# Performance work log

Measured on AMD Instinct MI355X. Metric: run time of the kernel, lower is better.

The kernel has to match this reference:

```python
import jax, jax.numpy as jnp
import numpy as np
from jax.scipy.special import digamma, gammaln

NUM_CLASSES = 3
FOCAL_GAMMA = 2.0
LABEL_SMOOTHING = 0.1
EVIDENTIAL_W = 0.1
CONTRASTIVE_W = 0.1
BOUNDARY_W = 0.15
TRIPLET_W = 0.1
QUALITY_W = 0.1
TRIPLET_MARGIN = 1.5


def setup_inputs() -> dict:
    key = jax.random.key(0)
    k1, k2, k3 = jax.random.split(key, 3)
    B, D = 4096, 512
    logits = jax.random.normal(k1, (B, NUM_CLASSES), dtype=jnp.float32)
    targets = jax.random.randint(k2, (B,), 0, 3)
    features = jax.random.normal(k3, (B, D), dtype=jnp.float32)
    alpha = jax.random.uniform(jax.random.fold_in(key, 7), (B, NUM_CLASSES), dtype=jnp.float32)
    focal_alpha = jnp.array([1.0, 2.0, 1.5], dtype=jnp.float32)
    class_weights = jnp.array([1.0, 2.0, 1.5], dtype=jnp.float32)
    return {"logits": logits, "targets": targets, "features": features,
            "alpha": alpha, "epoch": 1, "focal_alpha": focal_alpha,
            "class_weights": class_weights}


def reference(logits, targets, features, alpha, epoch, focal_alpha, class_weights):
    B = logits.shape[0]
    C = NUM_CLASSES

    # ---- focal loss (label-smoothed CE, torch semantics) ----
    logp = jax.nn.log_softmax(logits, axis=1)                      # [B,C]
    nll = -jnp.take_along_axis(logp, targets[:, None], axis=1)[:, 0]
    ce_ls = (1.0 - LABEL_SMOOTHING) * nll + LABEL_SMOOTHING * (-logp.mean(axis=1))
    pt = jnp.exp(-ce_ls)
    focal = (focal_alpha[targets] * (1.0 - pt) ** FOCAL_GAMMA * ce_ls).mean()

    # ---- weighted CE (torch weighted mean: sum(w*nll)/sum(w)) ----
    w = class_weights[targets]
    ce = (w * nll).sum() / w.sum()

    # ---- enhanced boundary loss ----
    probs = jax.nn.softmax(logits, axis=1)
    real = targets == 0
    semi = targets == 1
    syn = targets == 2
    rb = jnp.where(real, probs[:, 1] + 0.6 * probs[:, 2], 0.0).sum()
    sb = jnp.where(syn, probs[:, 1] + 0.4 * probs[:, 0], 0.0).sum()
    mb = jnp.where(semi, 1.0 - probs[:, 1] + 0.3 * (probs[:, 0] + probs[:, 2]), 0.0).sum()
    boundary = (rb + sb + 4.5 * mb) / (B + 1e-8)

    total = 0.4 * focal + 0.3 * ce + BOUNDARY_W * boundary

    # ---- normalized features and pairwise cosine-sim matrix ----
    norms = jnp.linalg.norm(features, axis=1, keepdims=True)
    f = features / jnp.maximum(norms, 1e-12)
    sim = f @ f.T                                                  # [B,B]
    same = targets[:, None] == targets[None, :]
    eye = jnp.eye(B, dtype=bool)

    # ---- enhanced contrastive loss ----
    pos = jnp.where(same, (1.0 - sim) ** 2, 0.0).sum()
    neg = jnp.where(~same, jnp.clip(sim - 0.2, 0.0) ** 2, 0.0).sum()
    semi_pair = semi[:, None] & semi[None, :]
    semi_l = jnp.where(semi_pair, (1.0 - sim) ** 2, 0.0).sum()
    contrastive = (pos + neg + 4.0 * semi_l) / (B * B + 1e-8)

    # ---- enhanced triplet loss (batch-hard, vectorized) ----
    d2 = jnp.clip(2.0 - 2.0 * sim, 0.0)
    dist = jnp.sqrt(jnp.where(eye, 1.0, d2))  # diag masked; safe sqrt
    pos_mask = same & ~eye
    neg_mask = ~same
    hp = jnp.max(jnp.where(pos_mask, dist, -jnp.inf), axis=1)
    hn = jnp.min(jnp.where(neg_mask, dist, jnp.inf), axis=1)
    valid = pos_mask.any(axis=1) & neg_mask.any(axis=1)
    margin = TRIPLET_MARGIN * jnp.where(targets == 1, 2.5, 1.0)
    tl = jax.nn.relu(hp - hn + margin)
    cnt = valid.sum()
    triplet = jnp.where(cnt > 0,
                        jnp.where(valid, tl, 0.0).sum() / jnp.maximum(cnt, 1),
                        0.0)

    # ---- quality-invariant loss (upper-tri same-class pairs) ----
    upper = jnp.triu(jnp.ones((B, B), dtype=bool), k=1)
    qmask = same & upper
    npairs = qmask.sum()
    q = jnp.where(qmask, (1.0 - sim) ** 2, 0.0).sum() / jnp.maximum(npairs, 1)
    frac2 = syn.astype(jnp.float32).mean()
    q = q * jnp.where(syn.sum() > 0, 1.0 + 2.5 * frac2, 1.0)
    quality = jnp.where(npairs > 0, q, 0.0)

    # ---- evidential loss ----
    onehot = jax.nn.one_hot(targets, C, dtype=jnp.float32)
    S = alpha.sum(axis=1, keepdims=True) + 1e-8
    likelihood = (onehot * (digamma(S) - digamma(alpha + 1e-8))).sum(axis=1)
    at = onehot + (1.0 - onehot) * alpha
    ats = at.sum(axis=1) + 1e-8
    kl = (gammaln(ats) - gammaln(at + 1e-8).sum(axis=1)
          + ((at - 1.0) * (digamma(at + 1e-8) - digamma(ats[:, None] + 1e-8))).sum(axis=1))
    annealing = min(1.0, (epoch / 25.0) ** 2)
    evidential = likelihood.mean() + annealing * 0.2 * kl.mean()

    total = (total + CONTRASTIVE_W * contrastive + TRIPLET_W * triplet
             + QUALITY_W * quality + EVIDENTIAL_W * evidential)
    return total
```

## Files before the change

### kernel.cpp

```cpp
#include <hip/hip_runtime.h>
#include <hip/hip_bf16.h>
#include <cstdint>

typedef __attribute__((ext_vector_type(8))) __bf16 bf8;
typedef __attribute__((ext_vector_type(4))) float f32x4;

#if defined(__has_builtin)
#if __has_builtin(__builtin_amdgcn_global_load_lds)
#define USE_GLL 1
#endif
#endif
#ifndef USE_GLL
#define USE_GLL 0
#endif

#if USE_GLL
__device__ __forceinline__ void gll16(const __bf16* g, __bf16* l){
  __builtin_amdgcn_global_load_lds(
      (const __attribute__((address_space(1))) void*)g,
      (__attribute__((address_space(3))) void*)l, 16, 0, 0);
}
#endif

__device__ __forceinline__ unsigned mapf(float x){
  unsigned u = __float_as_uint(x);
  return (u & 0x80000000u) ? ~u : (u | 0x80000000u);
}
__device__ __forceinline__ float unmapf(unsigned u){
  return __uint_as_float((u & 0x80000000u) ? (u & 0x7FFFFFFFu) : ~u);
}

__device__ float digammaf_(float x){
  float r = 0.f;
  while (x < 6.f){ r -= 1.f/x; x += 1.f; }
  float inv = 1.f/x, inv2 = inv*inv;
  r += logf(x) - 0.5f*inv
     - inv2*(0.08333333333f - inv2*(0.008333333333f - inv2*0.003968253968f));
  return r;
}

__global__ __launch_bounds__(256) void k_prep(const float* __restrict__ feat,
    __bf16* __restrict__ fb,
    const float* __restrict__ logits, const int* __restrict__ targets,
    const float* __restrict__ alpha,  const float* __restrict__ fa,
    const float* __restrict__ cw, int B, int D,
    float* __restrict__ psum, unsigned* __restrict__ pcnt,
    unsigned* rowMinU, unsigned* rowMaxU){
  int bid = blockIdx.x, tid = threadIdx.x;
  int wave = tid >> 6, lane = tid & 63;

  int row = bid*4 + wave;
  if (row < B){
    const float* src = feat + (size_t)row*D;
    float ss = 0.f;
    for (int c = lane*4; c < D; c += 64*4){
      float4 v = *(const float4*)(src + c);
      ss += v.x*v.x + v.y*v.y + v.z*v.z + v.w*v.w;
    }
    #pragma unroll
    for (int off=32; off; off>>=1) ss += __shfl_xor(ss, off);
    float inv = 1.f / fmaxf(sqrtf(ss), 1e-12f);
    __bf16* dst = fb + (size_t)row*D;
    for (int c = lane*8; c < D; c += 64*8){
      float4 v0 = *(const float4*)(src + c);
      float4 v1 = *(const float4*)(src + c + 4);
      bf8 o;
      o[0]=(__bf16)(v0.x*inv); o[1]=(__bf16)(v0.y*inv);
      o[2]=(__bf16)(v0.z*inv); o[3]=(__bf16)(v0.w*inv);
      o[4]=(__bf16)(v1.x*inv); o[5]=(__bf16)(v1.y*inv);
      o[6]=(__bf16)(v1.z*inv); o[7]=(__bf16)(v1.w*inv);
      *(bf8*)(dst + c) = o;
    }
  }

  int SB = B >> 8;
  if (bid >= SB) return;

  int i = bid*256 + tid;
  rowMinU[i] = 0xFFFFFFFFu; rowMaxU[i] = 0u;

  float l0=logits[3*i], l1=logits[3*i+1], l2=logits[3*i+2];
  int t = targets[i];
  float m = fmaxf(l0, fmaxf(l1,l2));
  float e0=expf(l0-m), e1=expf(l1-m), e2=expf(l2-m);
  float se = e0+e1+e2;
  float lse = m + logf(se);
  float lp0=l0-lse, lp1=l1-lse, lp2=l2-lse;
  float lpt = (t==0)?lp0:((t==1)?lp1:lp2);
  float nll = -lpt;
  float ce_ls = 0.9f*nll + 0.1f*(-(lp0+lp1+lp2)*(1.f/3.f));
  float pt = expf(-ce_ls);
  float om = 1.f - pt;
  float focal_i = fa[t]*om*om*ce_ls;
  float w = cw[t];
  float ce_n = w*nll, ce_d = w;
  float p0=e0/se, p1=e1/se, p2=e2/se;
  float bnd;
  if (t==0)      bnd = p1 + 0.6f*p2;
  else if (t==2) bnd = p1 + 0.4f*p0;
  else           bnd = 4.5f*(1.f - p1 + 0.3f*(p0+p2));
  float a0=alpha[3*i], a1=alpha[3*i+1], a2=alpha[3*i+2];
  float S = a0+a1+a2 + 1e-8f;
  float at_ = (t==0)?a0:((t==1)?a1:a2);
  float lik = digammaf_(S) - digammaf_(at_ + 1e-8f);
  float b0 = (t==0)?1.f:a0, b1 = (t==1)?1.f:a1, b2 = (t==2)?1.f:a2;
  float ats = b0+b1+b2 + 1e-8f;
  float psa = digammaf_(ats + 1e-8f);
  float kl = lgammaf(ats)
     - (lgammaf(b0+1e-8f)+lgammaf(b1+1e-8f)+lgammaf(b2+1e-8f))
     + (b0-1.f)*(digammaf_(b0+1e-8f)-psa)
     + (b1-1.f)*(digammaf_(b1+1e-8f)-psa)
     + (b2-1.f)*(digammaf_(b2+1e-8f)-psa);

  unsigned long long m0 = __ballot(t==0);
  unsigned long long m1 = __ballot(t==1);
  unsigned long long m2 = __ballot(t==2);
  #pragma unroll
  for (int off=32; off; off>>=1){
    focal_i += __shfl_xor(focal_i, off);
    ce_n    += __shfl_xor(ce_n, off);
    ce_d    += __shfl_xor(ce_d, off);
    bnd     += __shfl_xor(bnd, off);
    lik     += __shfl_xor(lik, off);
    kl      += __shfl_xor(kl, off);
  }
  if (lane == 0){
    int slot = bid*4 + wave;
    psum[slot*8+0]=focal_i; psum[slot*8+1]=ce_n; psum[slot*8+2]=ce_d;
    psum[slot*8+3]=bnd;     psum[slot*8+4]=lik;  psum[slot*8+5]=kl;
    pcnt[slot*4+0]=(unsigned)__popcll(m0);
    pcnt[slot*4+1]=(unsigned)__popcll(m1);
    pcnt[slot*4+2]=(unsigned)__popcll(m2);
  }
}

__global__ __launch_bounds__(64, 3) void k_pairs(const __bf16* __restrict__ fb,
    const int* __restrict__ targets, int B, int D,
    float* __restrict__ pairPart, unsigned* rowMinU, unsigned* rowMaxU){
  __shared__ __bf16 sA[2][2048];
  __shared__ __bf16 sB[2][2048];

  int t = blockIdx.x;
  int bx = (int)((sqrtf(8.f*(float)t + 1.f) - 1.f)*0.5f);
  while ((bx+1)*(bx+2)/2 <= t) bx++;
  while (bx*(bx+1)/2 > t) bx--;
  int by = t - bx*(bx+1)/2;
  bool isDiag = (by == bx);
  int rowBase = by*64, colBase = bx*64;

  int lane = threadIdx.x;
  int quad = lane >> 4, l16 = lane & 15;

  const __bf16* gA[4]; const __bf16* gB[4];
  #pragma unroll
  for (int j=0; j<4; j++){
    int row = j*16 + (lane >> 2);
    int gcb = (lane & 3) ^ ((row >> 1) & 3);
    gA[j] = fb + (size_t)(rowBase + row)*D + gcb*8;
    gB[j] = fb + (size_t)(colBase + row)*D + gcb*8;
  }

  int offA[4], offB[4];
  #pragma unroll
  for (int mi=0; mi<4; mi++){
    int R = mi*16 + l16;
    offA[mi] = R*32 + ((quad ^ ((R>>1)&3))*8);
    offB[mi] = offA[mi];
  }

  f32x4 C[4][4] = {};

#if USE_GLL
  #define STAGE(buf, k0) do{ \
    gll16(gA[0] + (k0), &sA[buf][0*512]); \
    gll16(gA[1] + (k0), &sA[buf][1*512]); \
    gll16(gA[2] + (k0), &sA[buf][2*512]); \
    gll16(gA[3] + (k0), &sA[buf][3*512]); \
    gll16(gB[0] + (k0), &sB[buf][0*512]); \
    gll16(gB[1] + (k0), &sB[buf][1*512]); \
    gll16(gB[2] + (k0), &sB[buf][2*512]); \
    gll16(gB[3] + (k0), &sB[buf][3*512]); \
  }while(0)
#else
  #define STAGE(buf, k0) do{ \
    _Pragma("unroll") \
    for (int j=0; j<4; j++){ \
      *(bf8*)&sA[buf][j*512 + lane*8] = *(const bf8*)(gA[j] + (k0)); \
      *(bf8*)&sB[buf][j*512 + lane*8] = *(const bf8*)(gB[j] + (k0)); \
    } \
  }while(0)
#endif

  #define COMPUTE(buf) do{ \
    bf8 aF[4], bF[4]; \
    _Pragma("unroll") \
    for (int mi=0; mi<4; mi++) aF[mi] = *(const bf8*)(&sA[buf][offA[mi]]); \
    _Pragma("unroll") \
    for (int ni=0; ni<4; ni++) bF[ni] = *(const bf8*)(&sB[buf][offB[ni]]); \
    _Pragma("unroll") \
    for (int mi=0; mi<4; mi++) \
      _Pragma("unroll") \
      for (int ni=0; ni<4; ni++) \
        C[mi][ni] = __builtin_amdgcn_mfma_f32_16x16x32_bf16(aF[mi], bF[ni], C[mi][ni], 0,0,0); \
  }while(0)

  int NIT = D/32;
  STAGE(0, 0);
  for (int it=0; it<NIT; it+=2){
    STAGE(1, (it+1)*32);
    COMPUTE(0);
    if (it+2 < NIT) STAGE(0, (it+2)*32);
    COMPUTE(1);
  }

  int tcol[4];
  #pragma unroll
  for (int ni=0; ni<4; ni++) tcol[ni] = targets[colBase + ni*16 + l16];

  float pos=0.f, neg=0.f, semi=0.f, diag=0.f;
  float cmin[4], cmax[4];
  #pragma unroll
  for (int ni=0; ni<4; ni++){ cmin[ni]=2.f; cmax[ni]=-2.f; }

  #pragma unroll
  for (int mi=0; mi<4; mi++){
    #pragma unroll
    for (int r=0; r<4; r++){
      int rl = mi*16 + quad*4 + r;
      int row = rowBase + rl;
      int tr = targets[row];
      float vmin = 2.f, vmax = -2.f;
      #pragma unroll
      for (int ni=0; ni<4; ni++){
        int col = colBase + ni*16 + l16;
        float s = C[mi][ni][r];
        if (tr == tcol[ni]){
          float omv = 1.f - s;
          float q = omv*omv;
          pos += q;
          if (tr == 1) semi += q;
          if (row == col) diag += q;
          else {
            vmin = fminf(vmin, s);
            cmin[ni] = fminf(cmin[ni], s);
          }
        } else {
          float c0 = fmaxf(s - 0.2f, 0.f);
          neg += c0*c0;
          vmax = fmaxf(vmax, s);
          cmax[ni] = fmaxf(cmax[ni], s);
        }
      }
      #pragma unroll
      for (int off=1; off<16; off<<=1){
        vmin = fminf(vmin, __shfl_xor(vmin, off));
        vmax = fmaxf(vmax, __shfl_xor(vmax, off));
      }
      if (l16 == 0){
        atomicMin(&rowMinU[row], mapf(vmin));
        atomicMax(&rowMaxU[row], mapf(vmax));
      }
    }
  }

  if (!isDiag){
    #pragma unroll
    for (int ni=0; ni<4; ni++){
      float cn = cmin[ni], cx = cmax[ni];
      cn = fminf(cn, __shfl_xor(cn, 16)); cn = fminf(cn, __shfl_xor(cn, 32));
      cx = fmaxf(cx, __shfl_xor(cx, 16)); cx = fmaxf(cx, __shfl_xor(cx, 32));
      if (quad == 0){
        int col = colBase + ni*16 + l16;
        atomicMin(&rowMinU[col], mapf(cn));
        atomicMax(&rowMaxU[col], mapf(cx));
      }
    }
  }

  #pragma unroll
  for (int off=32; off; off>>=1){
    pos  += __shfl_xor(pos, off);
    neg  += __shfl_xor(neg, off);
    semi += __shfl_xor(semi, off);
    diag += __shfl_xor(diag, off);
  }
  if (lane == 0){
    float fac = isDiag ? 1.f : 2.f;
    pairPart[blockIdx.x*4+0] = pos*fac;
    pairPart[blockIdx.x*4+1] = neg*fac;
    pairPart[blockIdx.x*4+2] = semi*fac;
    pairPart[blockIdx.x*4+3] = diag;
  }
}

__global__ __launch_bounds__(256) void k_final(const int* __restrict__ targets,
    const int* __restrict__ epoch_p, int B, int SB, int nblk,
    const float* __restrict__ pairPart, const float* __restrict__ psum,
    const unsigned* __restrict__ pcnt,
    const unsigned* rowMinU, const unsigned* rowMaxU, float* out){
  __shared__ float tot[6];
  __shared__ unsigned cn[3];
  __shared__ float ptot[4];
  int tid = threadIdx.x;
  int nslots = SB*4;
  int wave = tid>>6, lane = tid&63;

  if (tid < 64){
    float v0=0,v1=0,v2=0,v3=0,v4=0,v5=0;
    int c0=0,c1=0,c2=0;
    for (int s=tid; s<nslots; s+=64){
      v0+=psum[s*8+0]; v1+=psum[s*8+1]; v2+=psum[s*8+2];
      v3+=psum[s*8+3]; v4+=psum[s*8+4]; v5+=psum[s*8+5];
      c0+=(int)pcnt[s*4+0]; c1+=(int)pcnt[s*4+1]; c2+=(int)pcnt[s*4+2];
    }
    #pragma unroll
    for (int off=32; off; off>>=1){
      v0+=__shfl_xor(v0,off); v1+=__shfl_xor(v1,off); v2+=__shfl_xor(v2,off);
      v3+=__shfl_xor(v3,off); v4+=__shfl_xor(v4,off); v5+=__shfl_xor(v5,off);
      c0+=__shfl_xor(c0,off); c1+=__shfl_xor(c1,off); c2+=__shfl_xor(c2,off);
    }
    if (tid == 0){
      tot[0]=v0; tot[1]=v1; tot[2]=v2; tot[3]=v3; tot[4]=v4; tot[5]=v5;
      cn[0]=(unsigned)c0; cn[1]=(unsigned)c1; cn[2]=(unsigned)c2;
    }
  }

  {
    float p=0,n=0,s2=0,d=0;
    for (int s=tid; s<nblk; s+=256){
      p += pairPart[s*4+0]; n += pairPart[s*4+1];
      s2+= pairPart[s*4+2]; d += pairPart[s*4+3];
    }
    #pragma unroll
    for (int off=32; off; off>>=1){
      p+=__shfl_xor(p,off); n+=__shfl_xor(n,off);
      s2+=__shfl_xor(s2,off); d+=__shfl_xor(d,off);
    }
    __shared__ float pw[4][4];
    if (lane==0){ pw[wave][0]=p; pw[wave][1]=n; pw[wave][2]=s2; pw[wave][3]=d; }
    __syncthreads();
    if (tid==0){
      float a=0,b=0,c=0,e=0;
      for (int w2=0; w2<4; w2++){ a+=pw[w2][0]; b+=pw[w2][1]; c+=pw[w2][2]; e+=pw[w2][3]; }
      ptot[0]=a; ptot[1]=b; ptot[2]=c; ptot[3]=e;
    }
  }
  __syncthreads();
  int n0=(int)cn[0], n1=(int)cn[1], n2=(int)cn[2];

  float tsum = 0.f, tcnt = 0.f;
  for (int i = tid; i < B; i += 256){
    int t = targets[i];
    int nt = (t==0)?n0:((t==1)?n1:n2);
    if (nt - 1 > 0 && B - nt > 0){
      float mn = unmapf(rowMinU[i]);
      float mx = unmapf(rowMaxU[i]);
      float hp = sqrtf(fmaxf(2.f - 2.f*mn, 0.f));
      float hn = sqrtf(fmaxf(2.f - 2.f*mx, 0.f));
      float margin = 1.5f * ((t==1) ? 2.5f : 1.f);
      float tl = fmaxf(hp - hn + margin, 0.f);
      tsum += tl; tcnt += 1.f;
    }
  }
  #pragma unroll
  for (int off=32; off; off>>=1){ tsum += __shfl_xor(tsum, off); tcnt += __shfl_xor(tcnt, off); }
  __shared__ float sb[4][2];
  if (lane==0){ sb[wave][0]=tsum; sb[wave][1]=tcnt; }
  __syncthreads();
  if (tid==0){
    float ts=0, tn=0;
    for (int w2=0;w2<4;w2++){ ts+=sb[w2][0]; tn+=sb[w2][1]; }
    float triplet = (tn > 0.f) ? ts / fmaxf(tn, 1.f) : 0.f;
    float pos=ptot[0], neg=ptot[1], semi=ptot[2], diag=ptot[3];
    float Bf = (float)B;
    float focal = tot[0] / Bf;
    float ce = tot[1] / tot[2];
    float boundary = tot[3] / (Bf + 1e-8f);
    float contrastive = (pos + neg + 4.f*semi) / (Bf*Bf + 1e-8f);
    long long npl = ((long long)n0*(n0-1) + (long long)n1*(n1-1) + (long long)n2*(n2-1))/2;
    float qsum = (pos - diag) * 0.5f;
    float q = qsum / (float)(npl > 0 ? npl : 1);
    if (n2 > 0) q *= (1.f + 2.5f * ((float)n2 / Bf));
    float quality = (npl > 0) ? q : 0.f;
    int ep = epoch_p[0];
    float er = (float)ep / 25.f;
    float ann = fminf(1.f, er*er);
    float evidential = tot[4]/Bf + ann*0.2f*tot[5]/Bf;
    float total = 0.4f*focal + 0.3f*ce + 0.15f*boundary
                + 0.1f*contrastive + 0.1f*triplet + 0.1f*quality + 0.1f*evidential;
    out[0] = total;
  }
}

extern "C" void kernel_launch(void* const* d_in, const int* in_sizes, int n_in,
                              void* d_out, int out_size, void* d_ws, size_t ws_size,
                              hipStream_t stream){
  const float* logits   = (const float*)d_in[0];
  const int*   targets  = (const int*)d_in[1];
  const float* features = (const float*)d_in[2];
  const float* alpha    = (const float*)d_in[3];
  const int*   epoch    = (const int*)d_in[4];
  const float* fa       = (const float*)d_in[5];
  const float* cw       = (const float*)d_in[6];
  int B = in_sizes[1];
  int D = in_sizes[2] / B;
  int SB = B >> 8;
  int T  = B / 64;
  int nblk = T*(T+1)/2;

  char* ws = (char*)d_ws;
  unsigned* pcnt     = (unsigned*)(ws);
  float*    psum     = (float*)(ws + 16384);
  float*    pairPart = (float*)(ws + 32768);
  unsigned* rowMinU  = (unsigned*)(ws + 131072);
  unsigned* rowMaxU  = (unsigned*)(ws + 131072 + (size_t)B*4);
  __bf16*   fb       = (__bf16*)(ws + 131072 + (size_t)B*8);

  k_prep <<<B/4, 256, 0, stream>>>(features, fb, logits, targets, alpha, fa, cw,
                                   B, D, psum, pcnt, rowMinU, rowMaxU);
  k_pairs<<<nblk, 64, 0, stream>>>(fb, targets, B, D, pairPart, rowMinU, rowMaxU);
  k_final<<<1, 256, 0, stream>>>(targets, epoch, B, SB, nblk, pairPart, psum, pcnt,
                                 rowMinU, rowMaxU, (float*)d_out);
}
```

Baseline: 127.8 us.

## Pre-tile swizzled bf16 features, dedupe diagonal tile loads, widen final reduction

The prep kernel now writes normalized bf16 features in a tiled, pre-swizzled layout: one contiguous 64x32 chunk per tile and k-step. The pair kernel can then stream each chunk with fully contiguous loads instead of strided row gathers. Diagonal tiles load only the A operand and reuse it as B, and the occupancy hint on the pair kernel is removed. Per-row loss terms are now computed across all prep blocks with a block-level reduction. Class counts move into a 1024-thread final kernel that uses vectorized partial reads, which adds more partial slots to sum there.

```diff
diff --git a/kernel.cpp b/kernel.cpp
--- a/kernel.cpp
+++ b/kernel.cpp
@@ -40,45 +40,45 @@
 }
 
 __global__ __launch_bounds__(256) void k_prep(const float* __restrict__ feat,
-    __bf16* __restrict__ fb,
+    __bf16* __restrict__ fb2,
     const float* __restrict__ logits, const int* __restrict__ targets,
     const float* __restrict__ alpha,  const float* __restrict__ fa,
     const float* __restrict__ cw, int B, int D,
-    float* __restrict__ psum, unsigned* __restrict__ pcnt,
-    unsigned* rowMinU, unsigned* rowMaxU){
+    float* __restrict__ psum, unsigned* rowMinU, unsigned* rowMaxU){
   int bid = blockIdx.x, tid = threadIdx.x;
   int wave = tid >> 6, lane = tid & 63;
+  __shared__ float sloc[4][8];
 
   int row = bid*4 + wave;
-  if (row < B){
-    const float* src = feat + (size_t)row*D;
-    float ss = 0.f;
-    for (int c = lane*4; c < D; c += 64*4){
-      float4 v = *(const float4*)(src + c);
-      ss += v.x*v.x + v.y*v.y + v.z*v.z + v.w*v.w;
-    }
-    #pragma unroll
-    for (int off=32; off; off>>=1) ss += __shfl_xor(ss, off);
-    float inv = 1.f / fmaxf(sqrtf(ss), 1e-12f);
-    __bf16* dst = fb + (size_t)row*D;
-    for (int c = lane*8; c < D; c += 64*8){
-      float4 v0 = *(const float4*)(src + c);
-      float4 v1 = *(const float4*)(src + c + 4);
-      bf8 o;
-      o[0]=(__bf16)(v0.x*inv); o[1]=(__bf16)(v0.y*inv);
-      o[2]=(__bf16)(v0.z*inv); o[3]=(__bf16)(v0.w*inv);
-      o[4]=(__bf16)(v1.x*inv); o[5]=(__bf16)(v1.y*inv);
-      o[6]=(__bf16)(v1.z*inv); o[7]=(__bf16)(v1.w*inv);
-      *(bf8*)(dst + c) = o;
-    }
-  }
-
-  int SB = B >> 8;
-  if (bid >= SB) return;
-
-  int i = bid*256 + tid;
-  rowMinU[i] = 0xFFFFFFFFu; rowMaxU[i] = 0u;
-
+  const float* src = feat + (size_t)row*D;
+  float ss = 0.f;
+  for (int c = lane*4; c < D; c += 64*4){
+    float4 v = *(const float4*)(src + c);
+    ss += v.x*v.x + v.y*v.y + v.z*v.z + v.w*v.w;
+  }
+  #pragma unroll
+  for (int off=32; off; off>>=1) ss += __shfl_xor(ss, off);
+  float inv = 1.f / fmaxf(sqrtf(ss), 1e-12f);
+
+  int p = row >> 6, r = row & 63;
+  int rsw = (r >> 1) & 3;
+  for (int c = lane*8; c < D; c += 64*8){
+    float4 v0 = *(const float4*)(src + c);
+    float4 v1 = *(const float4*)(src + c + 4);
+    bf8 o;
+    o[0]=(__bf16)(v0.x*inv); o[1]=(__bf16)(v0.y*inv);
+    o[2]=(__bf16)(v0.z*inv); o[3]=(__bf16)(v0.w*inv);
+    o[4]=(__bf16)(v1.x*inv); o[5]=(__bf16)(v1.y*inv);
+    o[6]=(__bf16)(v1.z*inv); o[7]=(__bf16)(v1.w*inv);
+    int cc = c >> 5;
+    int cb = (c >> 3) & 3;
+    size_t off = (size_t)(p*16 + cc)*2048 + r*32 + ((cb ^ rsw)*8);
+    *(bf8*)(fb2 + off) = o;
+  }
+
+  if (tid < 4){ rowMinU[bid*4+tid] = 0xFFFFFFFFu; rowMaxU[bid*4+tid] = 0u; }
+
+  int i = row;
   float l0=logits[3*i], l1=logits[3*i+1], l2=logits[3*i+2];
   int t = targets[i];
   float m = fmaxf(l0, fmaxf(l1,l2));
@@ -111,30 +111,16 @@
      + (b0-1.f)*(digammaf_(b0+1e-8f)-psa)
      + (b1-1.f)*(digammaf_(b1+1e-8f)-psa)
      + (b2-1.f)*(digammaf_(b2+1e-8f)-psa);
-
-  unsigned long long m0 = __ballot(t==0);
-  unsigned long long m1 = __ballot(t==1);
-  unsigned long long m2 = __ballot(t==2);
-  #pragma unroll
-  for (int off=32; off; off>>=1){
-    focal_i += __shfl_xor(focal_i, off);
-    ce_n    += __shfl_xor(ce_n, off);
-    ce_d    += __shfl_xor(ce_d, off);
-    bnd     += __shfl_xor(bnd, off);
-    lik     += __shfl_xor(lik, off);
-    kl      += __shfl_xor(kl, off);
-  }
   if (lane == 0){
-    int slot = bid*4 + wave;
-    psum[slot*8+0]=focal_i; psum[slot*8+1]=ce_n; psum[slot*8+2]=ce_d;
-    psum[slot*8+3]=bnd;     psum[slot*8+4]=lik;  psum[slot*8+5]=kl;
-    pcnt[slot*4+0]=(unsigned)__popcll(m0);
-    pcnt[slot*4+1]=(unsigned)__popcll(m1);
-    pcnt[slot*4+2]=(unsigned)__popcll(m2);
-  }
-}
-
-__global__ __launch_bounds__(64, 3) void k_pairs(const __bf16* __restrict__ fb,
+    sloc[wave][0]=focal_i; sloc[wave][1]=ce_n; sloc[wave][2]=ce_d;
+    sloc[wave][3]=bnd;     sloc[wave][4]=lik;  sloc[wave][5]=kl;
+  }
+  __syncthreads();
+  if (tid < 6)
+    psum[bid*8+tid] = sloc[0][tid]+sloc[1][tid]+sloc[2][tid]+sloc[3][tid];
+}
+
+__global__ __launch_bounds__(64) void k_pairs(const __bf16* __restrict__ fb2,
     const int* __restrict__ targets, int B, int D,
     float* __restrict__ pairPart, unsigned* rowMinU, unsigned* rowMaxU){
   __shared__ __bf16 sA[2][2048];
@@ -150,43 +136,47 @@
 
   int lane = threadIdx.x;
   int quad = lane >> 4, l16 = lane & 15;
-
-  const __bf16* gA[4]; const __bf16* gB[4];
-  #pragma unroll
-  for (int j=0; j<4; j++){
-    int row = j*16 + (lane >> 2);
-    int gcb = (lane & 3) ^ ((row >> 1) & 3);
-    gA[j] = fb + (size_t)(rowBase + row)*D + gcb*8;
-    gB[j] = fb + (size_t)(colBase + row)*D + gcb*8;
-  }
-
-  int offA[4], offB[4];
+  int NCH = D/32;
+
+  const __bf16* srcA = fb2 + (size_t)by*NCH*2048 + lane*8;
+  const __bf16* srcB = fb2 + (size_t)bx*NCH*2048 + lane*8;
+  const __bf16* sB0  = isDiag ? &sA[0][0] : &sB[0][0];
+
+  int offA[4];
   #pragma unroll
   for (int mi=0; mi<4; mi++){
     int R = mi*16 + l16;
     offA[mi] = R*32 + ((quad ^ ((R>>1)&3))*8);
-    offB[mi] = offA[mi];
   }
 
   f32x4 C[4][4] = {};
 
 #if USE_GLL
-  #define STAGE(buf, k0) do{ \
-    gll16(gA[0] + (k0), &sA[buf][0*512]); \
-    gll16(gA[1] + (k0), &sA[buf][1*512]); \
-    gll16(gA[2] + (k0), &sA[buf][2*512]); \
-    gll16(gA[3] + (k0), &sA[buf][3*512]); \
-    gll16(gB[0] + (k0), &sB[buf][0*512]); \
-    gll16(gB[1] + (k0), &sB[buf][1*512]); \
-    gll16(gB[2] + (k0), &sB[buf][2*512]); \
-    gll16(gB[3] + (k0), &sB[buf][3*512]); \
+  #define STAGE(buf, it) do{ \
+    const __bf16* ga_ = srcA + (it)*2048; \
+    gll16(ga_ + 0*512, &sA[buf][0*512]); \
+    gll16(ga_ + 1*512, &sA[buf][1*512]); \
+    gll16(ga_ + 2*512, &sA[buf][2*512]); \
+    gll16(ga_ + 3*512, &sA[buf][3*512]); \
+    if (!isDiag){ \
+      const __bf16* gb_ = srcB + (it)*2048; \
+      gll16(gb_ + 0*512, &sB[buf][0*512]); \
+      gll16(gb_ + 1*512, &sB[buf][1*512]); \
+      gll16(gb_ + 2*512, &sB[buf][2*512]); \
+      gll16(gb_ + 3*512, &sB[buf][3*512]); \
+    } \
   }while(0)
 #else
-  #define STAGE(buf, k0) do{ \
+  #define STAGE(buf, it) do{ \
+    const __bf16* ga_ = srcA + (it)*2048; \
     _Pragma("unroll") \
-    for (int j=0; j<4; j++){ \
-      *(bf8*)&sA[buf][j*512 + lane*8] = *(const bf8*)(gA[j] + (k0)); \
-      *(bf8*)&sB[buf][j*512 + lane*8] = *(const bf8*)(gB[j] + (k0)); \
+    for (int j=0; j<4; j++) \
+      *(bf8*)&sA[buf][j*512 + lane*8] = *(const bf8*)(ga_ + j*512); \
+    if (!isDiag){ \
+      const __bf16* gb_ = srcB + (it)*2048; \
+      _Pragma("unroll") \
+      for (int j=0; j<4; j++) \
+        *(bf8*)&sB[buf][j*512 + lane*8] = *(const bf8*)(gb_ + j*512); \
     } \
   }while(0)
 #endif
@@ -194,9 +184,9 @@
   #define COMPUTE(buf) do{ \
     bf8 aF[4], bF[4]; \
     _Pragma("unroll") \
-    for (int mi=0; mi<4; mi++) aF[mi] = *(const bf8*)(&sA[buf][offA[mi]]); \
+    for (int mi=0; mi<4; mi++) aF[mi] = *(const bf8*)(&sA[0][0] + (buf)*2048 + offA[mi]); \
     _Pragma("unroll") \
-    for (int ni=0; ni<4; ni++) bF[ni] = *(const bf8*)(&sB[buf][offB[ni]]); \
+    for (int ni=0; ni<4; ni++) bF[ni] = *(const bf8*)(sB0 + (buf)*2048 + offA[ni]); \
     _Pragma("unroll") \
     for (int mi=0; mi<4; mi++) \
       _Pragma("unroll") \
@@ -204,12 +194,11 @@
         C[mi][ni] = __builtin_amdgcn_mfma_f32_16x16x32_bf16(aF[mi], bF[ni], C[mi][ni], 0,0,0); \
   }while(0)
 
-  int NIT = D/32;
   STAGE(0, 0);
-  for (int it=0; it<NIT; it+=2){
-    STAGE(1, (it+1)*32);
+  for (int it=0; it<NCH; it+=2){
+    STAGE(1, it+1);
     COMPUTE(0);
-    if (it+2 < NIT) STAGE(0, (it+2)*32);
+    if (it+2 < NCH) STAGE(0, it+2);
     COMPUTE(1);
   }
 
@@ -293,63 +282,86 @@
   }
 }
 
-__global__ __launch_bounds__(256) void k_final(const int* __restrict__ targets,
-    const int* __restrict__ epoch_p, int B, int SB, int nblk,
+__global__ __launch_bounds__(1024) void k_final(const int* __restrict__ targets,
+    const int* __restrict__ epoch_p, int B, int nprep, int nblk,
     const float* __restrict__ pairPart, const float* __restrict__ psum,
-    const unsigned* __restrict__ pcnt,
     const unsigned* rowMinU, const unsigned* rowMaxU, float* out){
-  __shared__ float tot[6];
-  __shared__ unsigned cn[3];
+  int tid = threadIdx.x, wave = tid>>6, lane = tid&63;
+  __shared__ float redf[16][8];
+  __shared__ int   redi[16][4];
+  __shared__ float tot6[6];
+  __shared__ int   cns[3];
   __shared__ float ptot[4];
-  int tid = threadIdx.x;
-  int nslots = SB*4;
-  int wave = tid>>6, lane = tid&63;
-
-  if (tid < 64){
+
+  {
+    int c0=0,c1=0,c2=0;
+    for (int i4 = tid; i4 < B/4; i4 += 1024){
+      int4 tv = ((const int4*)targets)[i4];
+      c0 += (tv.x==0)+(tv.y==0)+(tv.z==0)+(tv.w==0);
+      c1 += (tv.x==1)+(tv.y==1)+(tv.z==1)+(tv.w==1);
+      c2 += (tv.x==2)+(tv.y==2)+(tv.z==2)+(tv.w==2);
+    }
+    #pragma unroll
+    for (int off=32; off; off>>=1){
+      c0+=__shfl_xor(c0,off); c1+=__shfl_xor(c1,off); c2+=__shfl_xor(c2,off);
+    }
+    if (lane==0){ redi[wave][0]=c0; redi[wave][1]=c1; redi[wave][2]=c2; }
+  }
+  {
     float v0=0,v1=0,v2=0,v3=0,v4=0,v5=0;
-    int c0=0,c1=0,c2=0;
-    for (int s=tid; s<nslots; s+=64){
-      v0+=psum[s*8+0]; v1+=psum[s*8+1]; v2+=psum[s*8+2];
-      v3+=psum[s*8+3]; v4+=psum[s*8+4]; v5+=psum[s*8+5];
-      c0+=(int)pcnt[s*4+0]; c1+=(int)pcnt[s*4+1]; c2+=(int)pcnt[s*4+2];
+    for (int s = tid; s < nprep; s += 1024){
+      float4 a = *(const float4*)(psum + s*8);
+      float4 b = *(const float4*)(psum + s*8 + 4);
+      v0+=a.x; v1+=a.y; v2+=a.z; v3+=a.w; v4+=b.x; v5+=b.y;
     }
     #pragma unroll
     for (int off=32; off; off>>=1){
       v0+=__shfl_xor(v0,off); v1+=__shfl_xor(v1,off); v2+=__shfl_xor(v2,off);
       v3+=__shfl_xor(v3,off); v4+=__shfl_xor(v4,off); v5+=__shfl_xor(v5,off);
-      c0+=__shfl_xor(c0,off); c1+=__shfl_xor(c1,off); c2+=__shfl_xor(c2,off);
-    }
-    if (tid == 0){
-      tot[0]=v0; tot[1]=v1; tot[2]=v2; tot[3]=v3; tot[4]=v4; tot[5]=v5;
-      cn[0]=(unsigned)c0; cn[1]=(unsigned)c1; cn[2]=(unsigned)c2;
-    }
-  }
+    }
+    if (lane==0){
+      redf[wave][0]=v0; redf[wave][1]=v1; redf[wave][2]=v2;
+      redf[wave][3]=v3; redf[wave][4]=v4; redf[wave][5]=v5;
+    }
+  }
+  __syncthreads();
+  if (tid == 0){
+    int c0=0,c1=0,c2=0;
+    float v[6]={0,0,0,0,0,0};
+    for (int w2=0; w2<16; w2++){
+      c0+=redi[w2][0]; c1+=redi[w2][1]; c2+=redi[w2][2];
+      for (int j=0;j<6;j++) v[j]+=redf[w2][j];
+    }
+    cns[0]=c0; cns[1]=c1; cns[2]=c2;
+    for (int j=0;j<6;j++) tot6[j]=v[j];
+  }
+  __syncthreads();
 
   {
     float p=0,n=0,s2=0,d=0;
-    for (int s=tid; s<nblk; s+=256){
-      p += pairPart[s*4+0]; n += pairPart[s*4+1];
-      s2+= pairPart[s*4+2]; d += pairPart[s*4+3];
+    for (int s = tid; s < nblk; s += 1024){
+      float4 a = *(const float4*)(pairPart + s*4);
+      p+=a.x; n+=a.y; s2+=a.z; d+=a.w;
     }
     #pragma unroll
     for (int off=32; off; off>>=1){
       p+=__shfl_xor(p,off); n+=__shfl_xor(n,off);
       s2+=__shfl_xor(s2,off); d+=__shfl_xor(d,off);
     }
-    __shared__ float pw[4][4];
-    if (lane==0){ pw[wave][0]=p; pw[wave][1]=n; pw[wave][2]=s2; pw[wave][3]=d; }
-    __syncthreads();
-    if (tid==0){
-      float a=0,b=0,c=0,e=0;
-      for (int w2=0; w2<4; w2++){ a+=pw[w2][0]; b+=pw[w2][1]; c+=pw[w2][2]; e+=pw[w2][3]; }
-      ptot[0]=a; ptot[1]=b; ptot[2]=c; ptot[3]=e;
-    }
-  }
-  __syncthreads();
-  int n0=(int)cn[0], n1=(int)cn[1], n2=(int)cn[2];
+    if (lane==0){ redf[wave][0]=p; redf[wave][1]=n; redf[wave][2]=s2; redf[wave][3]=d; }
+  }
+  __syncthreads();
+  if (tid == 0){
+    float a=0,b=0,c=0,e=0;
+    for (int w2=0; w2<16; w2++){ a+=redf[w2][0]; b+=redf[w2][1]; c+=redf[w2][2]; e+=redf[w2][3]; }
+    ptot[0]=a; ptot[1]=b; ptot[2]=c; ptot[3]=e;
+  }
+  __syncthreads();
+
+  int n0=cns[0], n1=cns[1], n2=cns[2];
 
   float tsum = 0.f, tcnt = 0.f;
-  for (int i = tid; i < B; i += 256){
+  for (int i = tid; i < B; i += 1024){
     int t = targets[i];
     int nt = (t==0)?n0:((t==1)?n1:n2);
     if (nt - 1 > 0 && B - nt > 0){
@@ -364,18 +376,18 @@
   }
   #pragma unroll
   for (int off=32; off; off>>=1){ tsum += __shfl_xor(tsum, off); tcnt += __shfl_xor(tcnt, off); }
-  __shared__ float sb[4][2];
-  if (lane==0){ sb[wave][0]=tsum; sb[wave][1]=tcnt; }
-  __syncthreads();
+  if (lane==0){ redf[wave][6]=tsum; redf[wave][7]=tcnt; }
+  __syncthreads();
+
   if (tid==0){
     float ts=0, tn=0;
-    for (int w2=0;w2<4;w2++){ ts+=sb[w2][0]; tn+=sb[w2][1]; }
+    for (int w2=0; w2<16; w2++){ ts+=redf[w2][6]; tn+=redf[w2][7]; }
     float triplet = (tn > 0.f) ? ts / fmaxf(tn, 1.f) : 0.f;
     float pos=ptot[0], neg=ptot[1], semi=ptot[2], diag=ptot[3];
     float Bf = (float)B;
-    float focal = tot[0] / Bf;
-    float ce = tot[1] / tot[2];
-    float boundary = tot[3] / (Bf + 1e-8f);
+    float focal = tot6[0] / Bf;
+    float ce = tot6[1] / tot6[2];
+    float boundary = tot6[3] / (Bf + 1e-8f);
     float contrastive = (pos + neg + 4.f*semi) / (Bf*Bf + 1e-8f);
     long long npl = ((long long)n0*(n0-1) + (long long)n1*(n1-1) + (long long)n2*(n2-1))/2;
     float qsum = (pos - diag) * 0.5f;
@@ -385,7 +397,7 @@
     int ep = epoch_p[0];
     float er = (float)ep / 25.f;
     float ann = fminf(1.f, er*er);
-    float evidential = tot[4]/Bf + ann*0.2f*tot[5]/Bf;
+    float evidential = tot6[4]/Bf + ann*0.2f*tot6[5]/Bf;
     float total = 0.4f*focal + 0.3f*ce + 0.15f*boundary
                 + 0.1f*contrastive + 0.1f*triplet + 0.1f*quality + 0.1f*evidential;
     out[0] = total;
@@ -404,21 +416,20 @@
   const float* cw       = (const float*)d_in[6];
   int B = in_sizes[1];
   int D = in_sizes[2] / B;
-  int SB = B >> 8;
+  int nprep = B/4;
   int T  = B / 64;
   int nblk = T*(T+1)/2;
 
   char* ws = (char*)d_ws;
-  unsigned* pcnt     = (unsigned*)(ws);
-  float*    psum     = (float*)(ws + 16384);
-  float*    pairPart = (float*)(ws + 32768);
+  float*    psum     = (float*)(ws);
+  float*    pairPart = (float*)(ws + 65536);
   unsigned* rowMinU  = (unsigned*)(ws + 131072);
   unsigned* rowMaxU  = (unsigned*)(ws + 131072 + (size_t)B*4);
-  __bf16*   fb       = (__bf16*)(ws + 131072 + (size_t)B*8);
-
-  k_prep <<<B/4, 256, 0, stream>>>(features, fb, logits, targets, alpha, fa, cw,
-                                   B, D, psum, pcnt, rowMinU, rowMaxU);
-  k_pairs<<<nblk, 64, 0, stream>>>(fb, targets, B, D, pairPart, rowMinU, rowMaxU);
-  k_final<<<1, 256, 0, stream>>>(targets, epoch, B, SB, nblk, pairPart, psum, pcnt,
-                                 rowMinU, rowMaxU, (float*)d_out);
-}
+  __bf16*   fb2      = (__bf16*)(ws + 131072 + (size_t)B*8);
+
+  k_prep <<<nprep, 256, 0, stream>>>(features, fb2, logits, targets, alpha, fa, cw,
+                                     B, D, psum, rowMinU, rowMaxU);
+  k_pairs<<<nblk, 64, 0, stream>>>(fb2, targets, B, D, pairPart, rowMinU, rowMaxU);
+  k_final<<<1, 1024, 0, stream>>>(targets, epoch, B, nprep, nblk, pairPart, psum,
+                                  rowMinU, rowMaxU, (float*)d_out);
+}
```

New measurement: 120.0 us. -6.1%, faster.
